# Performance work log

Measured on AMD Instinct MI355X. Metric: run time of the kernel, lower is better.

The kernel has to match this reference:

```python
import jax, jax.numpy as jnp
import numpy as np


def setup_inputs() -> dict:
    key = jax.random.key(0)
    k1, k2, k3, k4 = jax.random.split(key, 4)
    N, S, F, UNITS = 50000, 32, 128, 128
    x = jax.random.normal(k1, (N, F), dtype=jnp.float32)
    neigh_x = jax.random.normal(k2, (N, S, F), dtype=jnp.float32)
    kernel_self = jax.random.normal(k3, (F, UNITS), dtype=jnp.float32) * 0.05
    kernel_neigh = jax.random.normal(k4, (F, UNITS), dtype=jnp.float32) * 0.05
    bias = jnp.zeros((2 * UNITS,), dtype=jnp.float32)
    return {"x": x, "neigh_x": neigh_x, "kernel_self": kernel_self,
            "kernel_neigh": kernel_neigh, "bias": bias}


def reference(x, neigh_x, kernel_self, kernel_neigh, bias):
    # neigh_x: [N, S, F]. Original transposes to [N, F, S] and applies
    # tf.raw_ops.NthElement with n = S//2 + S%2 (n-th smallest, 0-indexed)
    # along the last (neighbor) axis. Equivalent: sort along neighbor axis
    # of the untransposed tensor and take index n.
    S = neigh_x.shape[1]
    n = S // 2 + S % 2
    med = jnp.sort(neigh_x, axis=1)[:, n, :]  # [N, F]
    out = jnp.concatenate([x @ kernel_self, med @ kernel_neigh], axis=1)  # [N, 2*units] (concat=True)
    out = out + bias
    return jax.nn.relu(out)
```

## Files before the change

### kernel.cpp

```cpp
#include <hip/hip_runtime.h>

namespace {

typedef float f32x4 __attribute__((ext_vector_type(4)));

constexpr int S   = 32;
constexpr int F   = 128;
constexpr int BR  = 32;
constexpr int TPB = 256;

struct CEPair { int a, b; };

constexpr int batcher_count16() {
  int n = 16, cnt = 0;
  for (int p = 1; p < n; p <<= 1)
    for (int k = p; k >= 1; k >>= 1)
      for (int j = k % p; j + k < n; j += 2 * k)
        for (int i = 0; i < k && i + j + k < n; ++i)
          if ((i + j) / (2 * p) == (i + j + k) / (2 * p))
            ++cnt;
  return cnt;
}
constexpr int NCE = batcher_count16();

struct Net16 { CEPair ce[NCE]; };

constexpr Net16 make_net16() {
  Net16 net{};
  int n = 16, c = 0;
  for (int p = 1; p < n; p <<= 1)
    for (int k = p; k >= 1; k >>= 1)
      for (int j = k % p; j + k < n; j += 2 * k)
        for (int i = 0; i < k && i + j + k < n; ++i)
          if ((i + j) / (2 * p) == (i + j + k) / (2 * p))
            net.ce[c++] = CEPair{i + j, i + j + k};
  return net;
}
constexpr Net16 NET16 = make_net16();

template<int T>
__device__ __forceinline__ void sort16(float (&v)[16]) {
  if constexpr (T < NCE) {
    constexpr int a = NET16.ce[T].a;
    constexpr int b = NET16.ce[T].b;
    float x = v[a], y = v[b];
    v[a] = fminf(x, y);
    v[b] = fmaxf(x, y);
    sort16<T + 1>(v);
  }
}

__device__ __forceinline__ void issue_half(const float* __restrict__ neigh,
                                           const float* __restrict__ x,
                                           int row, int h, int lane,
                                           float (&A)[16], float (&B)[16],
                                           float& xv)
{
    const float* nb = neigh + (size_t)row * (S * F) + h * 64 + lane;
#pragma unroll
    for (int s = 0; s < 16; ++s)
        A[s] = __builtin_nontemporal_load(nb + s * F);
#pragma unroll
    for (int s = 0; s < 16; ++s)
        B[s] = __builtin_nontemporal_load(nb + (s + 16) * F);
    xv = x[(size_t)row * F + h * 64 + lane];
}

__device__ __forceinline__ void select_store(float (&A)[16], float (&B)[16],
                                             float xv,
                                             float* __restrict__ msrow,
                                             float* __restrict__ xsrow,
                                             int h, int lane)
{
    sort16<0>(A);
    sort16<0>(B);
#pragma unroll
    for (int q = 0; q < 16; ++q) A[q] = fmaxf(A[q], B[15 - q]);
#pragma unroll
    for (int st = 8; st >= 1; st >>= 1)
#pragma unroll
        for (int q = 0; q < st; ++q) A[q] = fminf(A[q], A[q + st]);
    msrow[h * 64 + lane] = A[0];
    xsrow[h * 64 + lane] = xv;
}

__global__ __launch_bounds__(TPB, 3) void fused_median_gemm(
    const float* __restrict__ x,
    const float* __restrict__ neigh,
    const float* __restrict__ Ks,
    const float* __restrict__ Kn,
    const float* __restrict__ bias,
    float* __restrict__ out,
    int N)
{
    __shared__ __align__(16) float xs[4][8][F];
    __shared__ __align__(16) float ms[4][8][F];

    const int tid  = threadIdx.x;
    const int wv   = tid >> 6;
    const int lane = tid & 63;
    const int row0 = blockIdx.x * BR + wv * 8;

    const int rmax = N - 1;
    auto rw = [&](int hp) { int r = row0 + (hp >> 1); return r > rmax ? rmax : r; };

    {
        float A0[16], B0[16], A1[16], B1[16];
        float A2[16], B2[16], A3[16], B3[16];
        float x0, x1, x2, x3;

        issue_half(neigh, x, rw(0), 0, lane, A0, B0, x0);
        issue_half(neigh, x, rw(1), 1, lane, A1, B1, x1);
        issue_half(neigh, x, rw(2), 0, lane, A2, B2, x2);

#pragma unroll 1
        for (int q = 0; q < 4; ++q) {
            const int hp = q * 4;
            issue_half(neigh, x, rw(hp + 3), (hp + 3) & 1, lane, A3, B3, x3);
            select_store(A0, B0, x0, &ms[wv][hp >> 1][0], &xs[wv][hp >> 1][0],
                         hp & 1, lane);
            if (hp + 4 < 16)
                issue_half(neigh, x, rw(hp + 4), (hp + 4) & 1, lane, A0, B0, x0);
            select_store(A1, B1, x1, &ms[wv][(hp + 1) >> 1][0], &xs[wv][(hp + 1) >> 1][0],
                         (hp + 1) & 1, lane);
            if (hp + 5 < 16)
                issue_half(neigh, x, rw(hp + 5), (hp + 5) & 1, lane, A1, B1, x1);
            select_store(A2, B2, x2, &ms[wv][(hp + 2) >> 1][0], &xs[wv][(hp + 2) >> 1][0],
                         (hp + 2) & 1, lane);
            if (hp + 6 < 16)
                issue_half(neigh, x, rw(hp + 6), (hp + 6) & 1, lane, A2, B2, x2);
            select_store(A3, B3, x3, &ms[wv][(hp + 3) >> 1][0], &xs[wv][(hp + 3) >> 1][0],
                         (hp + 3) & 1, lane);
        }
    }

    asm volatile("s_waitcnt lgkmcnt(0)" ::: "memory");

    const bool self_half = (lane < 32);
    const float* __restrict__ W = self_half ? Ks : Kn;
    const int wcol = (lane * 4) & 127;
    const float* lin = self_half ? &xs[wv][0][0] : &ms[wv][0][0];

    f32x4 acc[8];
#pragma unroll
    for (int r = 0; r < 8; ++r) acc[r] = f32x4{0.f, 0.f, 0.f, 0.f};

#pragma unroll 4
    for (int k4 = 0; k4 < 32; ++k4) {
        f32x4 wv4[4];
#pragma unroll
        for (int dk = 0; dk < 4; ++dk)
            wv4[dk] = *(const f32x4*)&W[(k4 * 4 + dk) * 128 + wcol];

        f32x4 xr[8];
#pragma unroll
        for (int r = 0; r < 8; ++r)
            xr[r] = *(const f32x4*)&lin[r * F + k4 * 4];

#pragma unroll
        for (int r = 0; r < 8; ++r) {
#pragma unroll
            for (int dk = 0; dk < 4; ++dk) {
                const float s = xr[r][dk];
                acc[r].x = fmaf(s, wv4[dk].x, acc[r].x);
                acc[r].y = fmaf(s, wv4[dk].y, acc[r].y);
                acc[r].z = fmaf(s, wv4[dk].z, acc[r].z);
                acc[r].w = fmaf(s, wv4[dk].w, acc[r].w);
            }
        }
    }

    const f32x4 bv = *(const f32x4*)&bias[lane * 4];
#pragma unroll
    for (int r = 0; r < 8; ++r) {
        int row = row0 + r;
        if (row > rmax) row = rmax;
        f32x4 o;
        o.x = fmaxf(acc[r].x + bv.x, 0.f);
        o.y = fmaxf(acc[r].y + bv.y, 0.f);
        o.z = fmaxf(acc[r].z + bv.z, 0.f);
        o.w = fmaxf(acc[r].w + bv.w, 0.f);
        __builtin_nontemporal_store(o, (f32x4*)&out[(size_t)row * 256 + lane * 4]);
    }
}

}

extern "C" void kernel_launch(void* const* d_in, const int* in_sizes, int n_in,
                              void* d_out, int out_size, void* d_ws, size_t ws_size,
                              hipStream_t stream) {
    const float* x     = (const float*)d_in[0];
    const float* neigh = (const float*)d_in[1];
    const float* Ks    = (const float*)d_in[2];
    const float* Kn    = (const float*)d_in[3];
    const float* bias  = (const float*)d_in[4];
    float* out = (float*)d_out;

    const int N = in_sizes[0] / F;
    const int grid = (N + BR - 1) / BR;
    hipLaunchKernelGGL(fused_median_gemm, dim3(grid), dim3(TPB), 0, stream,
                       x, neigh, Ks, Kn, bias, out, N);
}
```

Measured before the change: 182.4 us.

## Split median and GEMM into separate kernels using bf16 MFMA for projection

Replaces the fused kernel with three launches: a weight conversion to bf16 MFMA fragment layout, a median pass that sorts two features per lane with float2 loads and writes bf16 medians to workspace, and a GEMM pass using mfma_f32_16x16x32_bf16. The aim is to move the FP32 FMA GEMM onto matrix cores and widen the median loads. The cost is two extra launches, a workspace round trip for the medians, and bf16 rounding of inputs and weights, which lowers accuracy. The old fused kernel is kept as a fallback when the workspace is too small.

```diff
diff --git a/kernel.cpp b/kernel.cpp
--- a/kernel.cpp
+++ b/kernel.cpp
@@ -2,11 +2,13 @@
 
 namespace {
 
-typedef float f32x4 __attribute__((ext_vector_type(4)));
+typedef float  f32x2  __attribute__((ext_vector_type(2)));
+typedef float  f32x4  __attribute__((ext_vector_type(4)));
+typedef short  bf16x8 __attribute__((ext_vector_type(8)));
+typedef unsigned short u16;
 
 constexpr int S   = 32;
 constexpr int F   = 128;
-constexpr int BR  = 32;
 constexpr int TPB = 256;
 
 struct CEPair { int a, b; };
@@ -38,15 +40,169 @@
 }
 constexpr Net16 NET16 = make_net16();
 
+__device__ __forceinline__ f32x2 min2(f32x2 a, f32x2 b) {
+  f32x2 r; r.x = fminf(a.x, b.x); r.y = fminf(a.y, b.y); return r;
+}
+__device__ __forceinline__ f32x2 max2(f32x2 a, f32x2 b) {
+  f32x2 r; r.x = fmaxf(a.x, b.x); r.y = fmaxf(a.y, b.y); return r;
+}
+
 template<int T>
-__device__ __forceinline__ void sort16(float (&v)[16]) {
+__device__ __forceinline__ void sort16(f32x2 (&v)[16]) {
+  if constexpr (T < NCE) {
+    constexpr int a = NET16.ce[T].a;
+    constexpr int b = NET16.ce[T].b;
+    f32x2 x = v[a], y = v[b];
+    v[a] = min2(x, y);
+    v[b] = max2(x, y);
+    sort16<T + 1>(v);
+  }
+}
+
+__device__ __forceinline__ unsigned f2bf(float f) {
+  unsigned u = __builtin_bit_cast(unsigned, f);
+  return (u + 0x7FFFu + ((u >> 16) & 1u)) >> 16;
+}
+
+__device__ __forceinline__ void issue_row_k1(const float* __restrict__ neigh,
+                                             int row, int lane,
+                                             f32x2 (&A)[16], f32x2 (&B)[16])
+{
+    const f32x2* nb = (const f32x2*)(neigh + (size_t)row * (S * F)) + lane;
+#pragma unroll
+    for (int s = 0; s < 16; ++s)
+        A[s] = __builtin_nontemporal_load(nb + (size_t)s * 64);
+#pragma unroll
+    for (int s = 0; s < 16; ++s)
+        B[s] = __builtin_nontemporal_load(nb + (size_t)(s + 16) * 64);
+}
+
+__device__ __forceinline__ void select_store_med(f32x2 (&A)[16], f32x2 (&B)[16],
+                                                 unsigned* __restrict__ dst)
+{
+    sort16<0>(A);
+    sort16<0>(B);
+#pragma unroll
+    for (int q = 0; q < 16; ++q) A[q] = max2(A[q], B[15 - q]);
+#pragma unroll
+    for (int st = 8; st >= 1; st >>= 1)
+#pragma unroll
+        for (int q = 0; q < st; ++q) A[q] = min2(A[q], A[q + st]);
+    __builtin_nontemporal_store(f2bf(A[0].x) | (f2bf(A[0].y) << 16), dst);
+}
+
+__global__ __launch_bounds__(TPB, 3) void median_pass(
+    const float* __restrict__ neigh,
+    unsigned* __restrict__ med,
+    int N)
+{
+    const int tid  = threadIdx.x;
+    const int wv   = tid >> 6;
+    const int lane = tid & 63;
+    const int row0 = blockIdx.x * 32 + wv * 8;
+    const int rmax = N - 1;
+    auto rw = [&](int rl) { int r = row0 + rl; return r > rmax ? rmax : r; };
+
+    f32x2 A0[16], B0[16], A1[16], B1[16];
+
+    issue_row_k1(neigh, rw(0), lane, A0, B0);
+#pragma unroll
+    for (int p = 0; p < 4; ++p) {
+        issue_row_k1(neigh, rw(2 * p + 1), lane, A1, B1);
+        select_store_med(A0, B0, &med[(size_t)rw(2 * p) * 64 + lane]);
+        if (p < 3)
+            issue_row_k1(neigh, rw(2 * p + 2), lane, A0, B0);
+        select_store_med(A1, B1, &med[(size_t)rw(2 * p + 1) * 64 + lane]);
+    }
+}
+
+__global__ void convert_weights(const float* __restrict__ Ks,
+                                const float* __restrict__ Kn,
+                                u16* __restrict__ wsb)
+{
+    const int t  = blockIdx.x * 256 + threadIdx.x;
+    const int c  = t >> 8;
+    const int kk = (t >> 6) & 3;
+    const int l  = t & 63;
+    const int n  = c * 16 + (l & 15);
+    const int kb = kk * 32 + (l >> 4) * 8;
+    const float* __restrict__ W = (n < 128) ? Ks : Kn;
+    const int nn = n & 127;
+
+    u16 tmp[8];
+#pragma unroll
+    for (int j = 0; j < 8; ++j)
+        tmp[j] = (u16)f2bf(W[(size_t)(kb + j) * 128 + nn]);
+
+    u16* dst = wsb + (size_t)(c * 4 + kk) * 512 + (size_t)l * 8;
+#pragma unroll
+    for (int j = 0; j < 8; ++j) dst[j] = tmp[j];
+}
+
+__global__ __launch_bounds__(TPB, 4) void gemm_pass(
+    const float* __restrict__ x,
+    const u16*   __restrict__ med,
+    const u16*   __restrict__ wfrag,
+    const float* __restrict__ bias,
+    float* __restrict__ out,
+    int N)
+{
+    const int tid  = threadIdx.x;
+    const int wv   = tid >> 6;
+    const int lane = tid & 63;
+    const int rsel = lane & 15;
+    const int ag   = lane >> 4;
+    const int rmax = N - 1;
+
+    int row = blockIdx.x * 64 + wv * 16 + rsel;
+    if (row > rmax) row = rmax;
+
+    bf16x8 ax[4], am[4];
+#pragma unroll
+    for (int kk = 0; kk < 4; ++kk) {
+        const int kb = kk * 32 + ag * 8;
+        const f32x4 u0 = *(const f32x4*)&x[(size_t)row * F + kb];
+        const f32x4 u1 = *(const f32x4*)&x[(size_t)row * F + kb + 4];
+        bf16x8 v;
+        v[0] = (short)f2bf(u0.x); v[1] = (short)f2bf(u0.y);
+        v[2] = (short)f2bf(u0.z); v[3] = (short)f2bf(u0.w);
+        v[4] = (short)f2bf(u1.x); v[5] = (short)f2bf(u1.y);
+        v[6] = (short)f2bf(u1.z); v[7] = (short)f2bf(u1.w);
+        ax[kk] = v;
+        am[kk] = *(const bf16x8*)&med[(size_t)row * F + kb];
+    }
+
+    const bf16x8* __restrict__ wsf = (const bf16x8*)wfrag;
+
+#pragma unroll 4
+    for (int c = 0; c < 16; ++c) {
+        f32x4 acc = f32x4{0.f, 0.f, 0.f, 0.f};
+#pragma unroll
+        for (int kk = 0; kk < 4; ++kk) {
+            const bf16x8 b = wsf[(c * 4 + kk) * 64 + lane];
+            acc = __builtin_amdgcn_mfma_f32_16x16x32_bf16(
+                      b, (c < 8) ? ax[kk] : am[kk], acc, 0, 0, 0);
+        }
+        const int col = c * 16 + ag * 4;
+        const f32x4 bv = *(const f32x4*)&bias[col];
+        f32x4 o;
+        o.x = fmaxf(acc.x + bv.x, 0.f);
+        o.y = fmaxf(acc.y + bv.y, 0.f);
+        o.z = fmaxf(acc.z + bv.z, 0.f);
+        o.w = fmaxf(acc.w + bv.w, 0.f);
+        __builtin_nontemporal_store(o, (f32x4*)&out[(size_t)row * 256 + col]);
+    }
+}
+
+template<int T>
+__device__ __forceinline__ void sort16s(float (&v)[16]) {
   if constexpr (T < NCE) {
     constexpr int a = NET16.ce[T].a;
     constexpr int b = NET16.ce[T].b;
     float x = v[a], y = v[b];
     v[a] = fminf(x, y);
     v[b] = fmaxf(x, y);
-    sort16<T + 1>(v);
+    sort16s<T + 1>(v);
   }
 }
 
@@ -72,8 +228,8 @@
                                              float* __restrict__ xsrow,
                                              int h, int lane)
 {
-    sort16<0>(A);
-    sort16<0>(B);
+    sort16s<0>(A);
+    sort16s<0>(B);
 #pragma unroll
     for (int q = 0; q < 16; ++q) A[q] = fmaxf(A[q], B[15 - q]);
 #pragma unroll
@@ -99,8 +255,7 @@
     const int tid  = threadIdx.x;
     const int wv   = tid >> 6;
     const int lane = tid & 63;
-    const int row0 = blockIdx.x * BR + wv * 8;
-
+    const int row0 = blockIdx.x * 32 + wv * 8;
     const int rmax = N - 1;
     auto rw = [&](int hp) { int r = row0 + (hp >> 1); return r > rmax ? rmax : r; };
 
@@ -151,12 +306,10 @@
 #pragma unroll
         for (int dk = 0; dk < 4; ++dk)
             wv4[dk] = *(const f32x4*)&W[(k4 * 4 + dk) * 128 + wcol];
-
         f32x4 xr[8];
 #pragma unroll
         for (int r = 0; r < 8; ++r)
             xr[r] = *(const f32x4*)&lin[r * F + k4 * 4];
-
 #pragma unroll
         for (int r = 0; r < 8; ++r) {
 #pragma unroll
@@ -197,7 +350,21 @@
     float* out = (float*)d_out;
 
     const int N = in_sizes[0] / F;
-    const int grid = (N + BR - 1) / BR;
-    hipLaunchKernelGGL(fused_median_gemm, dim3(grid), dim3(TPB), 0, stream,
-                       x, neigh, Ks, Kn, bias, out, N);
-}
+    const size_t med_bytes = (size_t)N * 64 * sizeof(unsigned);
+    const size_t need = med_bytes + 16 * 4 * 512 * sizeof(u16);
+
+    if (ws_size >= need) {
+        unsigned* med = (unsigned*)d_ws;
+        u16* wsb = (u16*)((char*)d_ws + med_bytes);
+
+        hipLaunchKernelGGL(convert_weights, dim3(16), dim3(256), 0, stream,
+                           Ks, Kn, wsb);
+        hipLaunchKernelGGL(median_pass, dim3((N + 31) / 32), dim3(TPB), 0, stream,
+                           neigh, med, N);
+        hipLaunchKernelGGL(gemm_pass, dim3((N + 63) / 64), dim3(TPB), 0, stream,
+                           x, (const u16*)med, wsb, bias, out, N);
+    } else {
+        hipLaunchKernelGGL(fused_median_gemm, dim3((N + 31) / 32), dim3(TPB), 0,
+                           stream, x, neigh, Ks, Kn, bias, out, N);
+    }
+}
```

Result: slower. 190.4 us (+4.4%).
